# Performance work log

Measured on AMD Instinct MI355X. Metric: run time of the kernel, lower is better.

The kernel has to match this reference:

```python
import jax, jax.numpy as jnp
import numpy as np

N, E, H, C = 50000, 800000, 4, 32   # nodes, edges, heads, per-head channels
HID, LAT, G = H * C, 32, 128        # hidden, latent, num graphs
IN_DIM = 64
NEG_SLOPE = 0.2
BN_EPS = 1e-5


def setup_inputs() -> dict:
    key = jax.random.key(0)
    ks = jax.random.split(key, 20)
    inp = {
        "x": jax.random.normal(ks[0], (N, IN_DIM), jnp.float32),
        "edge_index": jax.random.randint(ks[1], (2, E), 0, N, jnp.int32),
        "batch": jnp.sort(jax.random.randint(ks[2], (N,), 0, G, jnp.int32)),
        # layer 0
        "W0": jax.random.normal(ks[3], (IN_DIM, HID), jnp.float32) * (1.0 / np.sqrt(IN_DIM)),
        "a_src0": jax.random.normal(ks[4], (H, C), jnp.float32) * 0.1,
        "a_dst0": jax.random.normal(ks[5], (H, C), jnp.float32) * 0.1,
        "b0": jnp.zeros((HID,), jnp.float32),
        # layer 1
        "W1": jax.random.normal(ks[6], (HID, HID), jnp.float32) * (1.0 / np.sqrt(HID)),
        "a_src1": jax.random.normal(ks[7], (H, C), jnp.float32) * 0.1,
        "a_dst1": jax.random.normal(ks[8], (H, C), jnp.float32) * 0.1,
        "b1": jnp.zeros((HID,), jnp.float32),
        # layer 2
        "W2": jax.random.normal(ks[9], (HID, HID), jnp.float32) * (1.0 / np.sqrt(HID)),
        "a_src2": jax.random.normal(ks[10], (H, C), jnp.float32) * 0.1,
        "a_dst2": jax.random.normal(ks[11], (H, C), jnp.float32) * 0.1,
        "b2": jnp.zeros((HID,), jnp.float32),
        # head
        "fc_w": jax.random.normal(ks[12], (HID, LAT), jnp.float32) * (1.0 / np.sqrt(HID)),
        "fc_b": jnp.zeros((LAT,), jnp.float32),
        "bn_g": jnp.ones((LAT,), jnp.float32),
        "bn_b": jnp.zeros((LAT,), jnp.float32),
    }
    return inp


def _gat_conv(x, src, dst, W, a_src, a_dst, b):
    n = x.shape[0]
    h = (x @ W).reshape(n, H, C)                      # [N,H,C]
    alpha_s = jnp.einsum("nhc,hc->nh", h, a_src)       # [N,H]
    alpha_d = jnp.einsum("nhc,hc->nh", h, a_dst)
    e = jax.nn.leaky_relu(alpha_s[src] + alpha_d[dst], NEG_SLOPE)  # [E',H]
    # scatter-softmax over incoming edges of each dst node
    m = jax.ops.segment_max(e, dst, num_segments=n)
    m = jnp.where(jnp.isfinite(m), m, 0.0)
    ex = jnp.exp(e - m[dst])
    denom = jax.ops.segment_sum(ex, dst, num_segments=n)
    alpha = ex / (denom[dst] + 1e-16)                  # [E',H]
    out = jax.ops.segment_sum(alpha[:, :, None] * h[src], dst, num_segments=n)
    return out.reshape(n, H * C) + b


def reference(x, edge_index, batch, W0, a_src0, a_dst0, b0, W1, a_src1, a_dst1, b1,
              W2, a_src2, a_dst2, b2, fc_w, fc_b, bn_g, bn_b):
    # PyG GATConv default add_self_loops=True
    loop = jnp.arange(N, dtype=edge_index.dtype)
    src = jnp.concatenate([edge_index[0], loop])
    dst = jnp.concatenate([edge_index[1], loop])

    h = x
    for (W, a_s, a_d, b) in ((W0, a_src0, a_dst0, b0),
                             (W1, a_src1, a_dst1, b1),
                             (W2, a_src2, a_dst2, b2)):
        h = _gat_conv(h, src, dst, W, a_s, a_d, b)
        h = jax.nn.leaky_relu(h, NEG_SLOPE)  # dropout is identity in eval

    pooled = jax.ops.segment_sum(h, batch, num_segments=G)  # global_add_pool -> [G,HID]
    out = pooled @ fc_w + fc_b
    # BatchNorm1d in eval mode with running_mean=0, running_var=1
    out = bn_g * out * (1.0 / np.sqrt(1.0 + BN_EPS)) + bn_b
    return out
```

## Files before the change

### kernel.cpp

```cpp
#include <hip/hip_runtime.h>
#include <hip/hip_bf16.h>
#include <float.h>

#define NEG 0.2f
#define SEGSHIFT 13

__device__ __forceinline__ float leaky(float x) { return x > 0.0f ? x : NEG * x; }

__device__ __forceinline__ unsigned short f2bf(float f) {
  unsigned x = __float_as_uint(f);
  unsigned r = (x + 0x7fffu + ((x >> 16) & 1u)) >> 16;
  return (unsigned short)r;
}

__device__ __forceinline__ float2 bf2f2(unsigned u) {
  float2 r;
  r.x = __uint_as_float(u << 16);
  r.y = __uint_as_float(u & 0xffff0000u);
  return r;
}

using frag8 = __attribute__((ext_vector_type(8))) short;
using f32x4v = __attribute__((ext_vector_type(4))) float;

__global__ void zero_kernel(int* __restrict__ p, int n) {
  int i = blockIdx.x * blockDim.x + threadIdx.x;
  int stride = gridDim.x * blockDim.x;
  for (; i < n; i += stride) p[i] = 0;
}

__global__ void wcvt_kernel(const float* __restrict__ W, unsigned short* __restrict__ Wt, int K) {
  int i = blockIdx.x * 256 + threadIdx.x;
  if (i >= K * 128) return;
  int k = i >> 7, n = i & 127;
  Wt[n * K + k] = f2bf(W[i]);
}

__global__ void count_kernel(const int* __restrict__ ei, int* __restrict__ degseg,
                             int E, int N, int nseg) {
  int i = blockIdx.x * blockDim.x + threadIdx.x;
  if (i >= E + N) return;
  int src, dst;
  if (i < E) { src = ei[i]; dst = ei[E + i]; } else { src = dst = i - E; }
  atomicAdd(&degseg[(size_t)dst * nseg + (src >> SEGSHIFT)], 1);
}

__global__ __launch_bounds__(1024) void scan_block_kernel(const int* __restrict__ deg,
                                                          int* __restrict__ row_start,
                                                          int* __restrict__ sums, int n) {
  __shared__ int buf[1024];
  int t = threadIdx.x;
  int idx = blockIdx.x * 1024 + t;
  int x = (idx < n) ? deg[idx] : 0;
  int v = x;
  buf[t] = v;
  __syncthreads();
  for (int off = 1; off < 1024; off <<= 1) {
    int a = (t >= off) ? buf[t - off] : 0;
    __syncthreads();
    v += a;
    buf[t] = v;
    __syncthreads();
  }
  if (idx < n) row_start[idx] = v - x;
  if (t == 1023) sums[blockIdx.x] = v;
}

__global__ __launch_bounds__(1024) void scan_sums_kernel(int* __restrict__ sums,
                                                         int* __restrict__ row_start,
                                                         int nch, int n) {
  __shared__ int buf[1024];
  int t = threadIdx.x;
  int x = (t < nch) ? sums[t] : 0;
  int v = x;
  buf[t] = v;
  __syncthreads();
  for (int off = 1; off < 1024; off <<= 1) {
    int a = (t >= off) ? buf[t - off] : 0;
    __syncthreads();
    v += a;
    buf[t] = v;
    __syncthreads();
  }
  if (t < nch) sums[t] = v - x;
  if (t == 1023) row_start[n] = v;
}

__global__ __launch_bounds__(1024) void scan_add_kernel(int* __restrict__ row_start,
                                                        const int* __restrict__ sums, int n) {
  int idx = blockIdx.x * 1024 + threadIdx.x;
  if (idx < n) row_start[idx] += sums[blockIdx.x];
}

__global__ void fill_kernel(const int* __restrict__ ei, int* __restrict__ cursor,
                            const int* __restrict__ rowseg, int* __restrict__ csr_src,
                            int E, int N, int nseg) {
  int i = blockIdx.x * blockDim.x + threadIdx.x;
  if (i >= E + N) return;
  int src, dst;
  if (i < E) { src = ei[i]; dst = ei[E + i]; } else { src = dst = i - E; }
  size_t b = (size_t)dst * nseg + (src >> SEGSHIFT);
  int pos = atomicAdd(&cursor[b], 1);
  csr_src[rowseg[b] + pos] = src;
}

template <int FP32IN>
__global__ __launch_bounds__(256) void gemm_kernel(const void* __restrict__ Xin,
                                                   const unsigned short* __restrict__ Wtg,
                                                   unsigned short* __restrict__ Hb,
                                                   const float* __restrict__ a_src,
                                                   const float* __restrict__ a_dst,
                                                   float* __restrict__ as_arr,
                                                   float* __restrict__ ad_arr,
                                                   int nrows, int K) {
  __shared__ unsigned short Wt[128][136];
  __shared__ unsigned short Xs[64][136];
  int t = threadIdx.x;
  int wave = t >> 6, lane = t & 63;
  int n0 = lane & 15, quad = lane >> 4;
  int row0 = blockIdx.x * 64, wrow = wave * 16;

  for (int idx = t; idx < (K * 128) / 8; idx += 256) {
    int n = idx / (K >> 3), c8 = idx % (K >> 3);
    *(uint4*)(&Wt[n][c8 * 8]) = *(const uint4*)(Wtg + (size_t)n * K + c8 * 8);
  }
  int rowElems = K >> 3;
  if (FP32IN) {
    const float* Xf = (const float*)Xin;
    for (int idx = t; idx < 64 * K; idx += 256) {
      int r = idx / K, k = idx % K;
      int gr = row0 + r;
      Xs[r][k] = f2bf(gr < nrows ? Xf[(size_t)gr * K + k] : 0.f);
    }
  } else {
    const unsigned short* Xb = (const unsigned short*)Xin;
    for (int idx = t; idx < 64 * rowElems; idx += 256) {
      int r = idx / rowElems, c8 = idx % rowElems;
      int gr = row0 + r;
      uint4 v = make_uint4(0, 0, 0, 0);
      if (gr < nrows) v = *(const uint4*)(Xb + (size_t)gr * K + c8 * 8);
      *(uint4*)(&Xs[r][c8 * 8]) = v;
    }
  }
  __syncthreads();

  f32x4v acc[8];
#pragma unroll
  for (int c = 0; c < 8; ++c) acc[c] = (f32x4v){0.f, 0.f, 0.f, 0.f};

  for (int kb = 0; kb < K; kb += 32) {
    frag8 a = *(const frag8*)(&Xs[wrow + n0][kb + quad * 8]);
#pragma unroll
    for (int c = 0; c < 8; ++c) {
      frag8 b = *(const frag8*)(&Wt[c * 16 + n0][kb + quad * 8]);
      acc[c] = __builtin_amdgcn_mfma_f32_16x16x32_bf16(a, b, acc[c], 0, 0, 0);
    }
  }

  float asv[8], adv[8];
#pragma unroll
  for (int c = 0; c < 8; ++c) {
    asv[c] = a_src[c * 16 + n0];
    adv[c] = a_dst[c * 16 + n0];
  }
#pragma unroll
  for (int r = 0; r < 4; ++r) {
    float ps[4] = {0.f, 0.f, 0.f, 0.f}, pd[4] = {0.f, 0.f, 0.f, 0.f};
#pragma unroll
    for (int c = 0; c < 8; ++c) {
      int h = c >> 1;
      ps[h] += acc[c][r] * asv[c];
      pd[h] += acc[c][r] * adv[c];
    }
#pragma unroll
    for (int off = 1; off < 16; off <<= 1) {
#pragma unroll
      for (int h = 0; h < 4; ++h) {
        ps[h] += __shfl_xor(ps[h], off);
        pd[h] += __shfl_xor(pd[h], off);
      }
    }
    if (n0 == 0) {
      int m = row0 + wrow + quad * 4 + r;
      if (m < nrows) {
#pragma unroll
        for (int h = 0; h < 4; ++h) {
          as_arr[(size_t)m * 4 + h] = ps[h];
          ad_arr[(size_t)m * 4 + h] = pd[h];
        }
      }
    }
  }

  __syncthreads();
#pragma unroll
  for (int c = 0; c < 8; ++c)
#pragma unroll
    for (int r = 0; r < 4; ++r)
      Xs[wrow + quad * 4 + r][c * 16 + n0] = f2bf(acc[c][r]);
  __syncthreads();
  for (int idx = t; idx < 64 * 16; idx += 256) {
    int r = idx >> 4, c8 = idx & 15;
    int gr = row0 + r;
    if (gr < nrows)
      *(uint4*)(Hb + (size_t)gr * 128 + c8 * 8) = *(const uint4*)(&Xs[r][c8 * 8]);
  }
}

template <int POOL>
__global__ __launch_bounds__(256) void agg_kernel(const unsigned short* __restrict__ Hb,
                                                  const float* __restrict__ as_arr,
                                                  const float* __restrict__ ad_arr,
                                                  const int* __restrict__ csr_src,
                                                  const int* __restrict__ rowseg,
                                                  const float* __restrict__ bias,
                                                  unsigned short* __restrict__ xnext,
                                                  const int* __restrict__ batch,
                                                  float* __restrict__ pooled,
                                                  int N, int nseg) {
  __shared__ int s_lds[4][64];
  __shared__ float e_lds[4][4][64];
  int wid = threadIdx.x >> 6;
  int lane = threadIdx.x & 63;
  int n = blockIdx.x * 4 + wid;
  if (n >= N) return;
  int rs = rowseg[(size_t)n * nseg];
  int re = rowseg[(size_t)n * nseg + nseg];
  int deg = re - rs;
  int l16 = lane & 15;
  int sub = lane >> 4;
  int head = l16 >> 2;

  float4 ad4 = *(const float4*)(ad_arr + (size_t)n * 4);
  const uint4* hb4 = (const uint4*)Hb;

  float4 dsum = make_float4(0.f, 0.f, 0.f, 0.f);
  float acc[8];
#pragma unroll
  for (int c = 0; c < 8; ++c) acc[c] = 0.f;

  for (int base = 0; base < deg; base += 64) {
    int cnt = min(64, deg - base);
    int s = 0;
    float4 e4 = make_float4(0.f, 0.f, 0.f, 0.f);
    if (lane < cnt) {
      s = csr_src[rs + base + lane];
      float4 a4 = *(const float4*)(as_arr + (size_t)s * 4);
      e4.x = __expf(fminf(leaky(a4.x + ad4.x), 80.f));
      e4.y = __expf(fminf(leaky(a4.y + ad4.y), 80.f));
      e4.z = __expf(fminf(leaky(a4.z + ad4.z), 80.f));
      e4.w = __expf(fminf(leaky(a4.w + ad4.w), 80.f));
    }
    dsum.x += e4.x; dsum.y += e4.y; dsum.z += e4.z; dsum.w += e4.w;
    s_lds[wid][lane] = s;
    e_lds[wid][0][lane] = e4.x;
    e_lds[wid][1][lane] = e4.y;
    e_lds[wid][2][lane] = e4.z;
    e_lds[wid][3][lane] = e4.w;

#pragma unroll 4
    for (int j = 0; j < cnt; j += 4) {
      int jj = j + sub;
      float ej = e_lds[wid][head][jj];
      int sj = s_lds[wid][jj];
      uint4 u = hb4[(size_t)sj * 16 + l16];
      float2 f;
      f = bf2f2(u.x); acc[0] += ej * f.x; acc[1] += ej * f.y;
      f = bf2f2(u.y); acc[2] += ej * f.x; acc[3] += ej * f.y;
      f = bf2f2(u.z); acc[4] += ej * f.x; acc[5] += ej * f.y;
      f = bf2f2(u.w); acc[6] += ej * f.x; acc[7] += ej * f.y;
    }
  }

#pragma unroll
  for (int c = 0; c < 8; ++c) acc[c] += __shfl_xor(acc[c], 16);
#pragma unroll
  for (int c = 0; c < 8; ++c) acc[c] += __shfl_xor(acc[c], 32);

#pragma unroll
  for (int off = 1; off < 64; off <<= 1) {
    dsum.x += __shfl_xor(dsum.x, off);
    dsum.y += __shfl_xor(dsum.y, off);
    dsum.z += __shfl_xor(dsum.z, off);
    dsum.w += __shfl_xor(dsum.w, off);
  }
  float denom = (head == 0) ? dsum.x : (head == 1) ? dsum.y : (head == 2) ? dsum.z : dsum.w;
  float inv = 1.0f / (denom + 1e-16f);

  if (POOL) {
    int g = batch[n];
    int c0 = 2 * sub;
    float v0 = leaky(acc[c0] * inv + bias[8 * l16 + c0]);
    float v1 = leaky(acc[c0 + 1] * inv + bias[8 * l16 + c0 + 1]);
    atomicAdd(&pooled[(size_t)g * 128 + 8 * l16 + c0], v0);
    atomicAdd(&pooled[(size_t)g * 128 + 8 * l16 + c0 + 1], v1);
  } else {
    if (sub == 0) {
      float4 bv0 = *(const float4*)(bias + 8 * l16);
      float4 bv1 = *(const float4*)(bias + 8 * l16 + 4);
      float v0 = leaky(acc[0] * inv + bv0.x);
      float v1 = leaky(acc[1] * inv + bv0.y);
      float v2 = leaky(acc[2] * inv + bv0.z);
      float v3 = leaky(acc[3] * inv + bv0.w);
      float v4 = leaky(acc[4] * inv + bv1.x);
      float v5 = leaky(acc[5] * inv + bv1.y);
      float v6 = leaky(acc[6] * inv + bv1.z);
      float v7 = leaky(acc[7] * inv + bv1.w);
      uint4 pk;
      pk.x = ((unsigned)f2bf(v1) << 16) | (unsigned)f2bf(v0);
      pk.y = ((unsigned)f2bf(v3) << 16) | (unsigned)f2bf(v2);
      pk.z = ((unsigned)f2bf(v5) << 16) | (unsigned)f2bf(v4);
      pk.w = ((unsigned)f2bf(v7) << 16) | (unsigned)f2bf(v6);
      ((uint4*)xnext)[(size_t)n * 16 + l16] = pk;
    }
  }
}

__global__ void head_kernel(const float* __restrict__ pooled, const float* __restrict__ fc_w,
                            const float* __restrict__ fc_b, const float* __restrict__ bn_g,
                            const float* __restrict__ bn_b, float* __restrict__ out, int G) {
  int t = threadIdx.x;
  int g = blockIdx.x * 8 + (t >> 5);
  int j = t & 31;
  if (g >= G) return;
  const float* pr = pooled + (size_t)g * 128;
  float acc = 0.f;
#pragma unroll 8
  for (int k = 0; k < 128; ++k) acc += pr[k] * fc_w[k * 32 + j];
  const float inv = 0.9999950000374997f;
  out[g * 32 + j] = bn_g[j] * (acc + fc_b[j]) * inv + bn_b[j];
}

extern "C" void kernel_launch(void* const* d_in, const int* in_sizes, int n_in,
                              void* d_out, int out_size, void* d_ws, size_t ws_size,
                              hipStream_t stream) {
  const float* x = (const float*)d_in[0];
  const int* ei = (const int*)d_in[1];
  const int* batch = (const int*)d_in[2];
  const float* Wm[3] = {(const float*)d_in[3], (const float*)d_in[7], (const float*)d_in[11]};
  const float* a_s[3] = {(const float*)d_in[4], (const float*)d_in[8], (const float*)d_in[12]};
  const float* a_d[3] = {(const float*)d_in[5], (const float*)d_in[9], (const float*)d_in[13]};
  const float* bb[3] = {(const float*)d_in[6], (const float*)d_in[10], (const float*)d_in[14]};
  const float* fc_w = (const float*)d_in[15];
  const float* fc_b = (const float*)d_in[16];
  const float* bn_g = (const float*)d_in[17];
  const float* bn_b = (const float*)d_in[18];
  float* out = (float*)d_out;

  int N = in_sizes[0] / 64;
  int E = in_sizes[1] / 2;
  int G = out_size / 32;
  int Etot = E + N;
  int nseg = ((N - 1) >> SEGSHIFT) + 1;
  int L = N * nseg;

  char* p = (char*)d_ws;
  auto carve = [&](size_t bytes) {
    char* r = p;
    p += (bytes + 255) & ~size_t(255);
    return r;
  };
  int* degseg    = (int*)carve((size_t)L * 4);
  int* cursor    = (int*)carve((size_t)L * 4);
  float* pooled  = (float*)carve((size_t)G * 128 * 4);
  int* rowseg    = (int*)carve((size_t)(L + 1) * 4);
  int* sums      = (int*)carve(4096);
  int* csr_src   = (int*)carve((size_t)Etot * 4);
  unsigned short* Hb  = (unsigned short*)carve((size_t)N * 128 * 2);
  unsigned short* Xb  = (unsigned short*)carve((size_t)N * 128 * 2);
  unsigned short* Wt0 = (unsigned short*)carve(64 * 128 * 2);
  unsigned short* Wt1 = (unsigned short*)carve(128 * 128 * 2);
  unsigned short* Wt2 = (unsigned short*)carve(128 * 128 * 2);
  float* as_arr  = (float*)carve((size_t)N * 4 * 4);
  float* ad_arr  = (float*)carve((size_t)N * 4 * 4);

  int nz = (int)(((char*)(pooled + (size_t)G * 128) - (char*)degseg) / 4);
  zero_kernel<<<512, 256, 0, stream>>>(degseg, nz);

  wcvt_kernel<<<(64 * 128 + 255) / 256, 256, 0, stream>>>(Wm[0], Wt0, 64);
  wcvt_kernel<<<(128 * 128 + 255) / 256, 256, 0, stream>>>(Wm[1], Wt1, 128);
  wcvt_kernel<<<(128 * 128 + 255) / 256, 256, 0, stream>>>(Wm[2], Wt2, 128);

  int egrid = (Etot + 255) / 256;
  count_kernel<<<egrid, 256, 0, stream>>>(ei, degseg, E, N, nseg);
  int nch = (L + 1023) / 1024;
  scan_block_kernel<<<nch, 1024, 0, stream>>>(degseg, rowseg, sums, L);
  scan_sums_kernel<<<1, 1024, 0, stream>>>(sums, rowseg, nch, L);
  scan_add_kernel<<<nch, 1024, 0, stream>>>(rowseg, sums, L);
  fill_kernel<<<egrid, 256, 0, stream>>>(ei, cursor, rowseg, csr_src, E, N, nseg);

  int ggrid = (N + 63) / 64;
  int ngrid = (N + 3) / 4;

  gemm_kernel<1><<<ggrid, 256, 0, stream>>>(x, Wt0, Hb, a_s[0], a_d[0], as_arr, ad_arr, N, 64);
  agg_kernel<0><<<ngrid, 256, 0, stream>>>(Hb, as_arr, ad_arr, csr_src, rowseg, bb[0],
                                           Xb, nullptr, nullptr, N, nseg);
  gemm_kernel<0><<<ggrid, 256, 0, stream>>>(Xb, Wt1, Hb, a_s[1], a_d[1], as_arr, ad_arr, N, 128);
  agg_kernel<0><<<ngrid, 256, 0, stream>>>(Hb, as_arr, ad_arr, csr_src, rowseg, bb[1],
                                           Xb, nullptr, nullptr, N, nseg);
  gemm_kernel<0><<<ggrid, 256, 0, stream>>>(Xb, Wt2, Hb, a_s[2], a_d[2], as_arr, ad_arr, N, 128);
  agg_kernel<1><<<ngrid, 256, 0, stream>>>(Hb, as_arr, ad_arr, csr_src, rowseg, bb[2],
                                           nullptr, batch, pooled, N, nseg);

  head_kernel<<<(G + 7) / 8, 256, 0, stream>>>(pooled, fc_w, fc_b, bn_g, bn_b, out, G);
}
```

Before: 471.0 us.

## Stage gathered neighbor rows into LDS via global_load_lds in edge chunks

The aggregation kernel now handles incoming edges in chunks of 24. For each chunk it issues asynchronous direct-to-LDS loads of the full 256-byte bf16 neighbor rows, using readlane to broadcast source indices, then accumulates from LDS. Before, each lane did a strided uint4 global gather per edge. This aims to raise memory-level parallelism and coalescing, at the cost of more LDS per block, full waits per chunk, and wasted loads for partial chunks. The pooling path also swaps dynamic acc indexing for a switch to avoid scratch spills.

```diff
diff --git a/kernel.cpp b/kernel.cpp
--- a/kernel.cpp
+++ b/kernel.cpp
@@ -4,6 +4,7 @@
 
 #define NEG 0.2f
 #define SEGSHIFT 13
+#define KE 24
 
 __device__ __forceinline__ float leaky(float x) { return x > 0.0f ? x : NEG * x; }
 
@@ -218,57 +219,62 @@
                                                   const int* __restrict__ batch,
                                                   float* __restrict__ pooled,
                                                   int N, int nseg) {
-  __shared__ int s_lds[4][64];
-  __shared__ float e_lds[4][4][64];
+  __shared__ __align__(16) char rowbuf[4][KE * 256];
+  __shared__ __align__(16) float e_lds[4][KE][4];
   int wid = threadIdx.x >> 6;
   int lane = threadIdx.x & 63;
   int n = blockIdx.x * 4 + wid;
   if (n >= N) return;
   int rs = rowseg[(size_t)n * nseg];
   int re = rowseg[(size_t)n * nseg + nseg];
-  int deg = re - rs;
   int l16 = lane & 15;
   int sub = lane >> 4;
   int head = l16 >> 2;
 
   float4 ad4 = *(const float4*)(ad_arr + (size_t)n * 4);
-  const uint4* hb4 = (const uint4*)Hb;
+  char* myrows = rowbuf[wid];
 
   float4 dsum = make_float4(0.f, 0.f, 0.f, 0.f);
   float acc[8];
 #pragma unroll
   for (int c = 0; c < 8; ++c) acc[c] = 0.f;
 
-  for (int base = 0; base < deg; base += 64) {
-    int cnt = min(64, deg - base);
-    int s = 0;
+  for (int base = rs; base < re; base += KE) {
+    asm volatile("s_waitcnt lgkmcnt(0)" ::: "memory");
+
+    int sj = 0;
     float4 e4 = make_float4(0.f, 0.f, 0.f, 0.f);
-    if (lane < cnt) {
-      s = csr_src[rs + base + lane];
-      float4 a4 = *(const float4*)(as_arr + (size_t)s * 4);
+    if (lane < KE && base + lane < re) {
+      sj = csr_src[base + lane];
+      float4 a4 = *(const float4*)(as_arr + (size_t)sj * 4);
       e4.x = __expf(fminf(leaky(a4.x + ad4.x), 80.f));
       e4.y = __expf(fminf(leaky(a4.y + ad4.y), 80.f));
       e4.z = __expf(fminf(leaky(a4.z + ad4.z), 80.f));
       e4.w = __expf(fminf(leaky(a4.w + ad4.w), 80.f));
-    }
-    dsum.x += e4.x; dsum.y += e4.y; dsum.z += e4.z; dsum.w += e4.w;
-    s_lds[wid][lane] = s;
-    e_lds[wid][0][lane] = e4.x;
-    e_lds[wid][1][lane] = e4.y;
-    e_lds[wid][2][lane] = e4.z;
-    e_lds[wid][3][lane] = e4.w;
-
-#pragma unroll 4
-    for (int j = 0; j < cnt; j += 4) {
-      int jj = j + sub;
-      float ej = e_lds[wid][head][jj];
-      int sj = s_lds[wid][jj];
-      uint4 u = hb4[(size_t)sj * 16 + l16];
+      dsum.x += e4.x; dsum.y += e4.y; dsum.z += e4.z; dsum.w += e4.w;
+    }
+    if (lane < KE) *(float4*)(&e_lds[wid][lane][0]) = e4;
+
+#pragma unroll
+    for (int j = 0; j < KE; ++j) {
+      int sju = __builtin_amdgcn_readlane(sj, j);
+      const char* gp = (const char*)Hb + (size_t)(unsigned)sju * 256 + lane * 4;
+      __builtin_amdgcn_global_load_lds(
+          (const __attribute__((address_space(1))) void*)gp,
+          (__attribute__((address_space(3))) void*)(myrows + j * 256), 4, 0, 0);
+    }
+    asm volatile("s_waitcnt vmcnt(0) lgkmcnt(0)" ::: "memory");
+    __builtin_amdgcn_sched_barrier(0);
+
+#pragma unroll
+    for (int j = 0; j < KE; j += 4) {
+      float w = e_lds[wid][j + sub][head];
+      uint4 u = *(const uint4*)(myrows + (j + sub) * 256 + l16 * 16);
       float2 f;
-      f = bf2f2(u.x); acc[0] += ej * f.x; acc[1] += ej * f.y;
-      f = bf2f2(u.y); acc[2] += ej * f.x; acc[3] += ej * f.y;
-      f = bf2f2(u.z); acc[4] += ej * f.x; acc[5] += ej * f.y;
-      f = bf2f2(u.w); acc[6] += ej * f.x; acc[7] += ej * f.y;
+      f = bf2f2(u.x); acc[0] += w * f.x; acc[1] += w * f.y;
+      f = bf2f2(u.y); acc[2] += w * f.x; acc[3] += w * f.y;
+      f = bf2f2(u.z); acc[4] += w * f.x; acc[5] += w * f.y;
+      f = bf2f2(u.w); acc[6] += w * f.x; acc[7] += w * f.y;
     }
   }
 
@@ -289,11 +295,18 @@
 
   if (POOL) {
     int g = batch[n];
-    int c0 = 2 * sub;
-    float v0 = leaky(acc[c0] * inv + bias[8 * l16 + c0]);
-    float v1 = leaky(acc[c0 + 1] * inv + bias[8 * l16 + c0 + 1]);
-    atomicAdd(&pooled[(size_t)g * 128 + 8 * l16 + c0], v0);
-    atomicAdd(&pooled[(size_t)g * 128 + 8 * l16 + c0 + 1], v1);
+    float p0 = 0.f, p1 = 0.f;
+    switch (sub) {
+      case 0: p0 = acc[0]; p1 = acc[1]; break;
+      case 1: p0 = acc[2]; p1 = acc[3]; break;
+      case 2: p0 = acc[4]; p1 = acc[5]; break;
+      case 3: p0 = acc[6]; p1 = acc[7]; break;
+    }
+    int ch = 8 * l16 + 2 * sub;
+    float v0 = leaky(p0 * inv + bias[ch]);
+    float v1 = leaky(p1 * inv + bias[ch + 1]);
+    atomicAdd(&pooled[(size_t)g * 128 + ch], v0);
+    atomicAdd(&pooled[(size_t)g * 128 + ch + 1], v1);
   } else {
     if (sub == 0) {
       float4 bv0 = *(const float4*)(bias + 8 * l16);
```

Result: slower. 502.3 us (+6.7%).
